# Optimization experiments

Measured on AMD Instinct MI355X. Metric: run time of the kernel, lower is better.

The kernel has to match this reference:

```python
import jax, jax.numpy as jnp
import numpy as np

EPS = 1e-6

def setup_inputs() -> dict:
    key = jax.random.key(0)
    k1, k2, k3 = jax.random.split(key, 3)
    B, N, D = 1, 2048, 1024
    x = jax.random.normal(k1, (B, N, D), dtype=jnp.float32)
    W_qvk = jax.random.normal(k2, (D, 3 * D), dtype=jnp.float32) * (D ** -0.5)
    b_qvk = jax.random.normal(k3, (3 * D,), dtype=jnp.float32) * 0.02
    return {"x": x, "W_qvk": W_qvk, "b_qvk": b_qvk, "head_num": 16}


def _forward(x, W_qvk, b_qvk, head_num):
    B, N, D = x.shape
    qvk = x @ W_qvk + b_qvk                       # (B, N, 3D)
    # torch.chunk order in source: q, v, k
    def to_heads(t):
        return t.reshape(B, N, head_num, D // head_num).transpose(0, 2, 1, 3)  # (B,h,N,e)
    q, v, k = (to_heads(t) for t in jnp.split(qvk, 3, axis=-1))
    e = q.shape[-1]
    # causal linear attention, bucket_size=1
    q = jax.nn.softmax(q, axis=-1) * (e ** -0.5)  # (B,h,N,e)
    k = jnp.exp(k)
    k_cumsum = jnp.cumsum(k, axis=2)              # (B,h,N,e)
    # per-position outer product k_i (x) v_i, then causal prefix-sum over N
    kv = jnp.einsum('bhnd,bhne->bhnde', k, v)     # (B,h,N,e,e)
    kv_cumsum = jnp.cumsum(kv, axis=2)            # (B,h,N,e,e)
    denom = jnp.einsum('bhnd,bhnd->bhn', q, k_cumsum + EPS)   # (B,h,N)
    out = jnp.einsum('bhnd,bhnde->bhne', q, kv_cumsum) / denom[..., None]
    # concat heads: (B,h,N,e) -> (B,N,D)
    return out.transpose(0, 2, 1, 3).reshape(B, N, D)


def reference(x, W_qvk, b_qvk, head_num):
    return _forward(x, W_qvk, b_qvk, head_num)
```

## Files before the change

### kernel.cpp

```cpp
#include <hip/hip_runtime.h>
#include <stdint.h>

#define NTOK 2048
#define NCH 32

typedef __attribute__((ext_vector_type(8))) short bf16x8;
typedef __attribute__((ext_vector_type(8))) unsigned short ushort8v;
typedef __attribute__((ext_vector_type(4))) float f32x4;

__device__ __forceinline__ unsigned short f2bf(float f) {
  unsigned u = __float_as_uint(f);
  u += 0x7fffu + ((u >> 16) & 1u);
  return (unsigned short)(u >> 16);
}
__device__ __forceinline__ float bf2f(unsigned short s) {
  return __uint_as_float(((unsigned)s) << 16);
}

__global__ __launch_bounds__(256) void k_prep_inputs(const float* __restrict__ x,
                                                     unsigned short* __restrict__ xb,
                                                     const float* __restrict__ W,
                                                     unsigned short* __restrict__ Wt) {
  int bid = blockIdx.x;
  if (bid < 2048) {
    int i = (bid * 256 + threadIdx.x) * 4;
    float4 v = *(const float4*)(x + i);
    ushort4 o = { f2bf(v.x), f2bf(v.y), f2bf(v.z), f2bf(v.w) };
    *(ushort4*)(xb + i) = o;
  } else {
    __shared__ float tile[32][33];
    int id = bid - 2048;
    int bx = id % 96, by = id / 96;
    int tx = threadIdx.x & 31, ty = threadIdx.x >> 5;
    int c0 = bx * 32;
    int r0 = by * 32;
#pragma unroll
    for (int j = 0; j < 32; j += 8)
      tile[ty + j][tx] = W[(size_t)(r0 + ty + j) * 3072 + c0 + tx];
    __syncthreads();
#pragma unroll
    for (int j = 0; j < 32; j += 8)
      Wt[(size_t)(c0 + ty + j) * 1024 + r0 + tx] = f2bf(tile[tx][ty + j]);
  }
}

__global__ __launch_bounds__(512, 4) void k_gemm_fused(const unsigned short* __restrict__ xb,
                                                       const unsigned short* __restrict__ wt,
                                                       const float* __restrict__ bias,
                                                       unsigned short* __restrict__ qh,
                                                       unsigned short* __restrict__ kh,
                                                       unsigned short* __restrict__ kt,
                                                       unsigned short* __restrict__ vt) {
  __shared__ __align__(16) unsigned short As[2][128][64];
  __shared__ __align__(16) unsigned short Bs[2][128][64];
  const int t = threadIdx.x;
  const int lane = t & 63;
  const int wave = t >> 6;
  const int wr = wave >> 1;
  const int wc = wave & 1;
  const int rowBase = blockIdx.y * 128;
  const int colBase = blockIdx.x * 128;
  const int fr = lane & 15;
  const int khalf = lane >> 4;

  const int sr = t >> 3;
  const int ssl = (t & 7) ^ (sr & 7);
  const unsigned short* agB = xb + (size_t)(rowBase + sr) * 1024 + ssl * 8;
  const unsigned short* bgB = wt + (size_t)(colBase + sr) * 1024 + ssl * 8;
  char* laB = (char*)As + t * 16;
  char* lbB = (char*)Bs + t * 16;

#define STG(buf, kt0) do {                                                                \
    _Pragma("unroll")                                                                     \
    for (int i_ = 0; i_ < 2; ++i_) {                                                      \
      __builtin_amdgcn_global_load_lds(                                                   \
          (const __attribute__((address_space(1))) void*)(agB + (kt0) * 64 + i_ * 65536), \
          (__attribute__((address_space(3))) void*)(laB + (buf) * 16384 + i_ * 8192), 16, 0, 0); \
      __builtin_amdgcn_global_load_lds(                                                   \
          (const __attribute__((address_space(1))) void*)(bgB + (kt0) * 64 + i_ * 65536), \
          (__attribute__((address_space(3))) void*)(lbB + (buf) * 16384 + i_ * 8192), 16, 0, 0); \
    }                                                                                     \
  } while (0)

#define VMCNT4() asm volatile("s_waitcnt vmcnt(4)" ::: "memory")
#define VMCNT0() asm volatile("s_waitcnt vmcnt(0)" ::: "memory")
#define LGKM0()  asm volatile("s_waitcnt lgkmcnt(0)" ::: "memory")
#define BAR()    __builtin_amdgcn_s_barrier()

  f32x4 acc[2][4] = {};
  const int fs0 = khalf ^ (fr & 7);

#define LOAD_FRAGS(cur, af, bff) do {                                                     \
    _Pragma("unroll")                                                                     \
    for (int m = 0; m < 2; ++m) {                                                         \
      const unsigned short* r = &As[cur][wr * 32 + m * 16 + fr][0];                       \
      af[m][0] = *(const bf16x8*)(r + fs0 * 8);                                           \
      af[m][1] = *(const bf16x8*)(r + (fs0 ^ 4) * 8);                                     \
    }                                                                                     \
    _Pragma("unroll")                                                                     \
    for (int n = 0; n < 4; ++n) {                                                         \
      const unsigned short* r = &Bs[cur][wc * 64 + n * 16 + fr][0];                       \
      bff[n][0] = *(const bf16x8*)(r + fs0 * 8);                                          \
      bff[n][1] = *(const bf16x8*)(r + (fs0 ^ 4) * 8);                                    \
    }                                                                                     \
  } while (0)

#define DO_MFMA(af, bff) do {                                                             \
    _Pragma("unroll")                                                                     \
    for (int m = 0; m < 2; ++m)                                                           \
      _Pragma("unroll")                                                                   \
      for (int n = 0; n < 4; ++n) {                                                       \
        acc[m][n] = __builtin_amdgcn_mfma_f32_16x16x32_bf16(af[m][0], bff[n][0], acc[m][n], 0, 0, 0); \
        acc[m][n] = __builtin_amdgcn_mfma_f32_16x16x32_bf16(af[m][1], bff[n][1], acc[m][n], 0, 0, 0); \
      }                                                                                   \
  } while (0)

  STG(0, 0);
  STG(1, 1);
#pragma unroll 1
  for (int ktile = 0; ktile < 14; ++ktile) {
    const int cur = ktile & 1;
    VMCNT4();
    BAR();
    bf16x8 af[2][2], bff[4][2];
    LOAD_FRAGS(cur, af, bff);
    LGKM0();
    __builtin_amdgcn_sched_barrier(0);
    BAR();
    STG(cur, ktile + 2);
    __builtin_amdgcn_s_setprio(1);
    DO_MFMA(af, bff);
    __builtin_amdgcn_s_setprio(0);
  }
  {
    VMCNT4();
    BAR();
    bf16x8 af[2][2], bff[4][2];
    LOAD_FRAGS(0, af, bff);
    DO_MFMA(af, bff);
  }
  {
    VMCNT0();
    BAR();
    bf16x8 af[2][2], bff[4][2];
    LOAD_FRAGS(1, af, bff);
    DO_MFMA(af, bff);
  }
#undef STG
#undef LOAD_FRAGS
#undef DO_MFMA

  const int g2 = khalf;
  const int ocol = lane & 15;
  const int col0 = colBase + wc * 64;
  const int region = col0 >> 10;
  const int h = (col0 & 1023) >> 6;
  const int r0 = rowBase + wr * 32;
  const int cch = r0 >> 6;
  const int lbase = (wr & 1) * 32;
  float bv[4];
#pragma unroll
  for (int n = 0; n < 4; ++n) bv[n] = bias[col0 + 16 * n + ocol];

  if (region == 0) {
#pragma unroll
    for (int m = 0; m < 2; ++m) {
#pragma unroll
      for (int i = 0; i < 4; ++i) {
        float v[4];
#pragma unroll
        for (int n = 0; n < 4; ++n) v[n] = acc[m][n][i] + bv[n];
        float mx = fmaxf(fmaxf(v[0], v[1]), fmaxf(v[2], v[3]));
#pragma unroll
        for (int off = 1; off <= 8; off <<= 1) mx = fmaxf(mx, __shfl_xor(mx, off));
        float s = 0.f;
#pragma unroll
        for (int n = 0; n < 4; ++n) { v[n] = __expf(v[n] - mx); s += v[n]; }
#pragma unroll
        for (int off = 1; off <= 8; off <<= 1) s += __shfl_xor(s, off);
        float inv = 0.125f / s;
        int tok = r0 + 16 * m + 4 * g2 + i;
        unsigned short* qrow = qh + ((size_t)h * NTOK + tok) * 64;
#pragma unroll
        for (int n = 0; n < 4; ++n) qrow[16 * n + ocol] = f2bf(v[n] * inv);
      }
    }
  } else if (region == 1) {
    unsigned short* vb = vt + (size_t)(h * NCH + cch) * 4096;
#pragma unroll
    for (int m = 0; m < 2; ++m) {
      int tl = lbase + 16 * m + 4 * g2;
#pragma unroll
      for (int n = 0; n < 4; ++n) {
        int e = 16 * n + ocol;
        ushort4 p = { f2bf(acc[m][n][0] + bv[n]), f2bf(acc[m][n][1] + bv[n]),
                      f2bf(acc[m][n][2] + bv[n]), f2bf(acc[m][n][3] + bv[n]) };
        *(ushort4*)&vb[(size_t)e * 64 + tl] = p;
      }
    }
  } else {
    unsigned short* kb = kt + (size_t)(h * NCH + cch) * 4096;
#pragma unroll
    for (int m = 0; m < 2; ++m) {
      int tl = lbase + 16 * m + 4 * g2;
#pragma unroll
      for (int n = 0; n < 4; ++n) {
        int e = 16 * n + ocol;
        float kv[4];
#pragma unroll
        for (int i = 0; i < 4; ++i) kv[i] = __expf(acc[m][n][i] + bv[n]);
        ushort4 p = { f2bf(kv[0]), f2bf(kv[1]), f2bf(kv[2]), f2bf(kv[3]) };
        *(ushort4*)&kb[(size_t)e * 64 + tl] = p;
#pragma unroll
        for (int i = 0; i < 4; ++i)
          kh[((size_t)h * NTOK + r0 + 16 * m + 4 * g2 + i) * 64 + e] = p[i];
      }
    }
  }
}

__global__ __launch_bounds__(256) void k_chunk_sums(const unsigned short* __restrict__ kt,
                                                    const unsigned short* __restrict__ vt,
                                                    float* __restrict__ Sc,
                                                    float* __restrict__ zc) {
  int h = blockIdx.x >> 5, c = blockIdx.x & 31;
  __shared__ __align__(16) unsigned short Kt[64][72], Vt[64][72];
  int t = threadIdx.x, lane = t & 63, w = t >> 6;
  int fr = lane & 15, g = lane >> 4, fko = g * 8;
  const unsigned short* kg = kt + (size_t)(h * NCH + c) * 4096;
  const unsigned short* vg = vt + (size_t)(h * NCH + c) * 4096;
  for (int s = t; s < 512; s += 256) {
    int r = s >> 3, c8 = (s & 7) * 8;
    *(ushort8v*)&Kt[r][c8] = *(const ushort8v*)&kg[r * 64 + c8];
    *(ushort8v*)&Vt[r][c8] = *(const ushort8v*)&vg[r * 64 + c8];
  }
  __syncthreads();
  bf16x8 ka[2];
#pragma unroll
  for (int ks = 0; ks < 2; ++ks) ka[ks] = *(const bf16x8*)&Kt[16 * w + fr][32 * ks + fko];
  f32x4 s4[4] = {};
#pragma unroll
  for (int nb = 0; nb < 4; ++nb)
#pragma unroll
    for (int ks = 0; ks < 2; ++ks) {
      bf16x8 vf = *(const bf16x8*)&Vt[16 * nb + fr][32 * ks + fko];
      s4[nb] = __builtin_amdgcn_mfma_f32_16x16x32_bf16(ka[ks], vf, s4[nb], 0, 0, 0);
    }
  float* so = Sc + (size_t)(h * NCH + c) * 4096;
#pragma unroll
  for (int nb = 0; nb < 4; ++nb) {
    float4 o = { s4[nb][0], s4[nb][1], s4[nb][2], s4[nb][3] };
    *(float4*)&so[(size_t)(16 * nb + fr) * 64 + 16 * w + 4 * g] = o;
  }
  if (w == 0) {
    float z = 0.f;
#pragma unroll
    for (int j = 0; j < 8; ++j) {
      bf16x8 kv = *(const bf16x8*)&Kt[lane][j * 8];
#pragma unroll
      for (int e = 0; e < 8; ++e) z += bf2f((unsigned short)kv[e]);
    }
    zc[(size_t)(h * NCH + c) * 64 + lane] = z;
  }
}

__global__ __launch_bounds__(256) void k_scan(const float* __restrict__ Sc,
                                              unsigned short* __restrict__ Sp,
                                              const float* __restrict__ zc,
                                              float* __restrict__ zp) {
  int b = blockIdx.x;
  if (b < 256) {
    int tg = b * 256 + threadIdx.x;
    int h = tg >> 12, e = tg & 4095;
    float run = 0.f;
    for (int c = 0; c < NCH; ++c) {
      size_t idx = (size_t)(h * NCH + c) * 4096 + e;
      float v = Sc[idx];
      Sp[idx] = f2bf(run);
      run += v;
    }
  } else {
#pragma unroll
    for (int j = 0; j < 4; ++j) {
      int s = threadIdx.x + j * 256;
      int h = s >> 6, d = s & 63;
      float run = 0.f;
      for (int c = 0; c < NCH; ++c) {
        size_t idx = (size_t)(h * NCH + c) * 64 + d;
        zp[idx] = run;
        run += zc[idx];
      }
    }
  }
}

__global__ __launch_bounds__(256) void k_attn(const unsigned short* __restrict__ qh,
                                              const unsigned short* __restrict__ kh,
                                              const unsigned short* __restrict__ vt,
                                              const unsigned short* __restrict__ Sp,
                                              const float* __restrict__ zp,
                                              float* __restrict__ out) {
  int h = blockIdx.x >> 5, c = blockIdx.x & 31;
  __shared__ __align__(16) unsigned short Qs[64][72], Ks[64][72], Vts[64][72], Sts[64][72], Ams[64][72];
  __shared__ float zs[64], denom[64];
  int t = threadIdx.x, lane = t & 63, w = t >> 6;
  int fr = lane & 15, g = lane >> 4, fko = g * 8;
  const unsigned short* qg = qh + ((size_t)h * NTOK + c * 64) * 64;
  const unsigned short* kg = kh + ((size_t)h * NTOK + c * 64) * 64;
  const unsigned short* vg = vt + (size_t)(h * NCH + c) * 4096;
  const unsigned short* sg = Sp + (size_t)(h * NCH + c) * 4096;
  for (int s = t; s < 512; s += 256) {
    int r = s >> 3, c8 = (s & 7) * 8;
    *(ushort8v*)&Qs[r][c8]  = *(const ushort8v*)&qg[r * 64 + c8];
    *(ushort8v*)&Ks[r][c8]  = *(const ushort8v*)&kg[r * 64 + c8];
    *(ushort8v*)&Vts[r][c8] = *(const ushort8v*)&vg[r * 64 + c8];
    *(ushort8v*)&Sts[r][c8] = *(const ushort8v*)&sg[r * 64 + c8];
  }
  if (t < 64) zs[t] = zp[(size_t)(h * NCH + c) * 64 + t];
  __syncthreads();

  bf16x8 qa[2];
#pragma unroll
  for (int ks = 0; ks < 2; ++ks) qa[ks] = *(const bf16x8*)&Qs[16 * w + fr][32 * ks + fko];
  f32x4 a1[4] = {};
#pragma unroll
  for (int mb = 0; mb < 4; ++mb)
#pragma unroll
    for (int ks = 0; ks < 2; ++ks) {
      bf16x8 kf = *(const bf16x8*)&Ks[16 * mb + fr][32 * ks + fko];
      a1[mb] = __builtin_amdgcn_mfma_f32_16x16x32_bf16(qa[ks], kf, a1[mb], 0, 0, 0);
    }
#pragma unroll
  for (int i = 0; i < 4; ++i) {
    int n = 16 * w + 4 * g + i;
    float rs = 0.f;
#pragma unroll
    for (int j = 0; j < 4; ++j) rs += bf2f(Qs[n][fr * 4 + j]) * zs[fr * 4 + j];
#pragma unroll
    for (int mb = 0; mb < 4; ++mb) {
      int m = 16 * mb + fr;
      float v = (m <= n) ? a1[mb][i] : 0.f;
      a1[mb][i] = v;
      rs += v;
      Ams[n][16 * mb + fr] = f2bf(v);
    }
#pragma unroll
    for (int off = 1; off <= 8; off <<= 1) rs += __shfl_xor(rs, off);
    if (fr == 0) denom[n] = rs + 1.25e-7f;
  }
  __syncthreads();

  bf16x8 xa[4];
#pragma unroll
  for (int ks = 0; ks < 2; ++ks) {
    xa[ks]     = *(const bf16x8*)&Vts[16 * w + fr][32 * ks + fko];
    xa[2 + ks] = *(const bf16x8*)&Sts[16 * w + fr][32 * ks + fko];
  }
  f32x4 o4[4] = {};
#pragma unroll
  for (int nb = 0; nb < 4; ++nb)
#pragma unroll
    for (int ks = 0; ks < 2; ++ks) {
      bf16x8 afr = *(const bf16x8*)&Ams[16 * nb + fr][32 * ks + fko];
      o4[nb] = __builtin_amdgcn_mfma_f32_16x16x32_bf16(xa[ks], afr, o4[nb], 0, 0, 0);
      bf16x8 qfr = *(const bf16x8*)&Qs[16 * nb + fr][32 * ks + fko];
      o4[nb] = __builtin_amdgcn_mfma_f32_16x16x32_bf16(xa[2 + ks], qfr, o4[nb], 0, 0, 0);
    }
#pragma unroll
  for (int nb = 0; nb < 4; ++nb) {
    int n = 16 * nb + fr;
    float dv = denom[n];
    float4 res = { o4[nb][0] / dv, o4[nb][1] / dv, o4[nb][2] / dv, o4[nb][3] / dv };
    *(float4*)&out[(size_t)(c * 64 + n) * 1024 + h * 64 + 16 * w + 4 * g] = res;
  }
}

extern "C" void kernel_launch(void* const* d_in, const int* in_sizes, int n_in,
                              void* d_out, int out_size, void* d_ws, size_t ws_size,
                              hipStream_t stream) {
  (void)in_sizes; (void)n_in; (void)out_size; (void)ws_size;
  const float* x = (const float*)d_in[0];
  const float* W = (const float*)d_in[1];
  const float* b = (const float*)d_in[2];
  char* ws = (char*)d_ws;

  const size_t MB = 1024 * 1024;
  unsigned short* xb = (unsigned short*)(ws + 0);
  unsigned short* Wt = (unsigned short*)(ws + 4 * MB);
  unsigned short* qh = (unsigned short*)(ws + 10 * MB);
  unsigned short* kh = (unsigned short*)(ws + 14 * MB);
  unsigned short* kt = (unsigned short*)(ws + 18 * MB);
  unsigned short* vt = (unsigned short*)(ws + 22 * MB);
  float*          Sc = (float*)(ws + 26 * MB);
  unsigned short* Sp = (unsigned short*)(ws + 34 * MB);
  float*          zc = (float*)(ws + 38 * MB);
  float*          zp = (float*)(ws + 38 * MB + 131072);

  k_prep_inputs<<<dim3(5120), dim3(256), 0, stream>>>(x, xb, W, Wt);
  k_gemm_fused<<<dim3(24, 16), dim3(512), 0, stream>>>(xb, Wt, b, qh, kh, kt, vt);
  k_chunk_sums<<<dim3(512), dim3(256), 0, stream>>>(kt, vt, Sc, zc);
  k_scan<<<dim3(257), dim3(256), 0, stream>>>(Sc, Sp, zc, zp);
  k_attn<<<dim3(512), dim3(256), 0, stream>>>(qh, kh, vt, Sp, zp, (float*)d_out);
}
```

Baseline: 48.41 us.

## Fold chunk-state prefix scan into attention kernel and store chunk sums in bf16

Drops the separate k_scan launch. Each attention block now sums the per-chunk KV states and z sums of all earlier chunks itself, reading bf16 chunk sums that k_chunk_sums now writes instead of fp32. This removes one kernel launch and the global round trip for the scanned prefix. In exchange there is redundant O(c) work per block, so later chunks read up to 31 chunk states, which causes load imbalance. Accumulation now happens over values already rounded to bf16, which adds some precision loss.

```diff
diff --git a/kernel.cpp b/kernel.cpp
--- a/kernel.cpp
+++ b/kernel.cpp
@@ -221,7 +221,7 @@
 
 __global__ __launch_bounds__(256) void k_chunk_sums(const unsigned short* __restrict__ kt,
                                                     const unsigned short* __restrict__ vt,
-                                                    float* __restrict__ Sc,
+                                                    unsigned short* __restrict__ Sc,
                                                     float* __restrict__ zc) {
   int h = blockIdx.x >> 5, c = blockIdx.x & 31;
   __shared__ __align__(16) unsigned short Kt[64][72], Vt[64][72];
@@ -246,11 +246,11 @@
       bf16x8 vf = *(const bf16x8*)&Vt[16 * nb + fr][32 * ks + fko];
       s4[nb] = __builtin_amdgcn_mfma_f32_16x16x32_bf16(ka[ks], vf, s4[nb], 0, 0, 0);
     }
-  float* so = Sc + (size_t)(h * NCH + c) * 4096;
+  unsigned short* so = Sc + (size_t)(h * NCH + c) * 4096;
 #pragma unroll
   for (int nb = 0; nb < 4; ++nb) {
-    float4 o = { s4[nb][0], s4[nb][1], s4[nb][2], s4[nb][3] };
-    *(float4*)&so[(size_t)(16 * nb + fr) * 64 + 16 * w + 4 * g] = o;
+    ushort4 o = { f2bf(s4[nb][0]), f2bf(s4[nb][1]), f2bf(s4[nb][2]), f2bf(s4[nb][3]) };
+    *(ushort4*)&so[(size_t)(16 * nb + fr) * 64 + 16 * w + 4 * g] = o;
   }
   if (w == 0) {
     float z = 0.f;
@@ -261,44 +261,14 @@
       for (int e = 0; e < 8; ++e) z += bf2f((unsigned short)kv[e]);
     }
     zc[(size_t)(h * NCH + c) * 64 + lane] = z;
-  }
-}
-
-__global__ __launch_bounds__(256) void k_scan(const float* __restrict__ Sc,
-                                              unsigned short* __restrict__ Sp,
-                                              const float* __restrict__ zc,
-                                              float* __restrict__ zp) {
-  int b = blockIdx.x;
-  if (b < 256) {
-    int tg = b * 256 + threadIdx.x;
-    int h = tg >> 12, e = tg & 4095;
-    float run = 0.f;
-    for (int c = 0; c < NCH; ++c) {
-      size_t idx = (size_t)(h * NCH + c) * 4096 + e;
-      float v = Sc[idx];
-      Sp[idx] = f2bf(run);
-      run += v;
-    }
-  } else {
-#pragma unroll
-    for (int j = 0; j < 4; ++j) {
-      int s = threadIdx.x + j * 256;
-      int h = s >> 6, d = s & 63;
-      float run = 0.f;
-      for (int c = 0; c < NCH; ++c) {
-        size_t idx = (size_t)(h * NCH + c) * 64 + d;
-        zp[idx] = run;
-        run += zc[idx];
-      }
-    }
   }
 }
 
 __global__ __launch_bounds__(256) void k_attn(const unsigned short* __restrict__ qh,
                                               const unsigned short* __restrict__ kh,
                                               const unsigned short* __restrict__ vt,
-                                              const unsigned short* __restrict__ Sp,
-                                              const float* __restrict__ zp,
+                                              const unsigned short* __restrict__ Sc,
+                                              const float* __restrict__ zc,
                                               float* __restrict__ out) {
   int h = blockIdx.x >> 5, c = blockIdx.x & 31;
   __shared__ __align__(16) unsigned short Qs[64][72], Ks[64][72], Vts[64][72], Sts[64][72], Ams[64][72];
@@ -308,15 +278,33 @@
   const unsigned short* qg = qh + ((size_t)h * NTOK + c * 64) * 64;
   const unsigned short* kg = kh + ((size_t)h * NTOK + c * 64) * 64;
   const unsigned short* vg = vt + (size_t)(h * NCH + c) * 4096;
-  const unsigned short* sg = Sp + (size_t)(h * NCH + c) * 4096;
   for (int s = t; s < 512; s += 256) {
     int r = s >> 3, c8 = (s & 7) * 8;
     *(ushort8v*)&Qs[r][c8]  = *(const ushort8v*)&qg[r * 64 + c8];
     *(ushort8v*)&Ks[r][c8]  = *(const ushort8v*)&kg[r * 64 + c8];
     *(ushort8v*)&Vts[r][c8] = *(const ushort8v*)&vg[r * 64 + c8];
-    *(ushort8v*)&Sts[r][c8] = *(const ushort8v*)&sg[r * 64 + c8];
-  }
-  if (t < 64) zs[t] = zp[(size_t)(h * NCH + c) * 64 + t];
+  }
+  {
+    float r[16] = {};
+    const unsigned short* sb = Sc + ((size_t)h * NCH) * 4096 + t * 16;
+    for (int cc = 0; cc < c; ++cc) {
+      ushort8v u0 = *(const ushort8v*)(sb + (size_t)cc * 4096);
+      ushort8v u1 = *(const ushort8v*)(sb + (size_t)cc * 4096 + 8);
+#pragma unroll
+      for (int j = 0; j < 8; ++j) { r[j] += bf2f(u0[j]); r[8 + j] += bf2f(u1[j]); }
+    }
+    ushort8v o0, o1;
+#pragma unroll
+    for (int j = 0; j < 8; ++j) { o0[j] = f2bf(r[j]); o1[j] = f2bf(r[8 + j]); }
+    int rr = t >> 2, ccol = (t & 3) * 16;
+    *(ushort8v*)&Sts[rr][ccol] = o0;
+    *(ushort8v*)&Sts[rr][ccol + 8] = o1;
+  }
+  if (t < 64) {
+    float z = 0.f;
+    for (int cc = 0; cc < c; ++cc) z += zc[((size_t)h * NCH + cc) * 64 + t];
+    zs[t] = z;
+  }
   __syncthreads();
 
   bf16x8 qa[2];
@@ -391,14 +379,11 @@
   unsigned short* kh = (unsigned short*)(ws + 14 * MB);
   unsigned short* kt = (unsigned short*)(ws + 18 * MB);
   unsigned short* vt = (unsigned short*)(ws + 22 * MB);
-  float*          Sc = (float*)(ws + 26 * MB);
-  unsigned short* Sp = (unsigned short*)(ws + 34 * MB);
-  float*          zc = (float*)(ws + 38 * MB);
-  float*          zp = (float*)(ws + 38 * MB + 131072);
+  unsigned short* Sc = (unsigned short*)(ws + 26 * MB);
+  float*          zc = (float*)(ws + 30 * MB);
 
   k_prep_inputs<<<dim3(5120), dim3(256), 0, stream>>>(x, xb, W, Wt);
   k_gemm_fused<<<dim3(24, 16), dim3(512), 0, stream>>>(xb, Wt, b, qh, kh, kt, vt);
   k_chunk_sums<<<dim3(512), dim3(256), 0, stream>>>(kt, vt, Sc, zc);
-  k_scan<<<dim3(257), dim3(256), 0, stream>>>(Sc, Sp, zc, zp);
-  k_attn<<<dim3(512), dim3(256), 0, stream>>>(qh, kh, vt, Sp, zp, (float*)d_out);
-}
+  k_attn<<<dim3(512), dim3(256), 0, stream>>>(qh, kh, vt, Sc, zc, (float*)d_out);
+}
```

Result: slower. 56.30 us (+16.3%).

## Fuse chunk-sum, scan and attention into one cooperative kernel with grid syncs

Applied to the files above, without the earlier changes.

Merges the three tail kernels (per-chunk KV sums, cross-chunk prefix scan, and chunked attention) into one cooperative kernel that uses grid-wide barriers in place of kernel boundaries. The per-chunk KV sums are now stored as bf16 instead of fp32, which halves that intermediate traffic. The aim is to remove two launch gaps and shrink memory traffic. In exchange it requires all 512 blocks to be co-resident, rounds the chunk sums to bf16 before the scan, and leaves most blocks idle during the scan phase.

```diff
diff --git a/kernel.cpp b/kernel.cpp
--- a/kernel.cpp
+++ b/kernel.cpp
@@ -1,5 +1,8 @@
 #include <hip/hip_runtime.h>
+#include <hip/hip_cooperative_groups.h>
 #include <stdint.h>
+
+namespace cg = cooperative_groups;
 
 #define NTOK 2048
 #define NCH 32
@@ -219,92 +222,88 @@
   }
 }
 
-__global__ __launch_bounds__(256) void k_chunk_sums(const unsigned short* __restrict__ kt,
-                                                    const unsigned short* __restrict__ vt,
-                                                    float* __restrict__ Sc,
-                                                    float* __restrict__ zc) {
-  int h = blockIdx.x >> 5, c = blockIdx.x & 31;
-  __shared__ __align__(16) unsigned short Kt[64][72], Vt[64][72];
-  int t = threadIdx.x, lane = t & 63, w = t >> 6;
-  int fr = lane & 15, g = lane >> 4, fko = g * 8;
-  const unsigned short* kg = kt + (size_t)(h * NCH + c) * 4096;
-  const unsigned short* vg = vt + (size_t)(h * NCH + c) * 4096;
-  for (int s = t; s < 512; s += 256) {
-    int r = s >> 3, c8 = (s & 7) * 8;
-    *(ushort8v*)&Kt[r][c8] = *(const ushort8v*)&kg[r * 64 + c8];
-    *(ushort8v*)&Vt[r][c8] = *(const ushort8v*)&vg[r * 64 + c8];
-  }
-  __syncthreads();
-  bf16x8 ka[2];
-#pragma unroll
-  for (int ks = 0; ks < 2; ++ks) ka[ks] = *(const bf16x8*)&Kt[16 * w + fr][32 * ks + fko];
-  f32x4 s4[4] = {};
-#pragma unroll
-  for (int nb = 0; nb < 4; ++nb)
-#pragma unroll
-    for (int ks = 0; ks < 2; ++ks) {
-      bf16x8 vf = *(const bf16x8*)&Vt[16 * nb + fr][32 * ks + fko];
-      s4[nb] = __builtin_amdgcn_mfma_f32_16x16x32_bf16(ka[ks], vf, s4[nb], 0, 0, 0);
-    }
-  float* so = Sc + (size_t)(h * NCH + c) * 4096;
-#pragma unroll
-  for (int nb = 0; nb < 4; ++nb) {
-    float4 o = { s4[nb][0], s4[nb][1], s4[nb][2], s4[nb][3] };
-    *(float4*)&so[(size_t)(16 * nb + fr) * 64 + 16 * w + 4 * g] = o;
-  }
-  if (w == 0) {
-    float z = 0.f;
-#pragma unroll
-    for (int j = 0; j < 8; ++j) {
-      bf16x8 kv = *(const bf16x8*)&Kt[lane][j * 8];
-#pragma unroll
-      for (int e = 0; e < 8; ++e) z += bf2f((unsigned short)kv[e]);
-    }
-    zc[(size_t)(h * NCH + c) * 64 + lane] = z;
-  }
-}
-
-__global__ __launch_bounds__(256) void k_scan(const float* __restrict__ Sc,
-                                              unsigned short* __restrict__ Sp,
-                                              const float* __restrict__ zc,
-                                              float* __restrict__ zp) {
-  int b = blockIdx.x;
-  if (b < 256) {
-    int tg = b * 256 + threadIdx.x;
-    int h = tg >> 12, e = tg & 4095;
-    float run = 0.f;
-    for (int c = 0; c < NCH; ++c) {
-      size_t idx = (size_t)(h * NCH + c) * 4096 + e;
-      float v = Sc[idx];
-      Sp[idx] = f2bf(run);
-      run += v;
-    }
-  } else {
-#pragma unroll
-    for (int j = 0; j < 4; ++j) {
-      int s = threadIdx.x + j * 256;
-      int h = s >> 6, d = s & 63;
-      float run = 0.f;
-      for (int c = 0; c < NCH; ++c) {
-        size_t idx = (size_t)(h * NCH + c) * 64 + d;
-        zp[idx] = run;
-        run += zc[idx];
-      }
-    }
-  }
-}
-
-__global__ __launch_bounds__(256) void k_attn(const unsigned short* __restrict__ qh,
-                                              const unsigned short* __restrict__ kh,
-                                              const unsigned short* __restrict__ vt,
-                                              const unsigned short* __restrict__ Sp,
-                                              const float* __restrict__ zp,
-                                              float* __restrict__ out) {
-  int h = blockIdx.x >> 5, c = blockIdx.x & 31;
+__global__ __launch_bounds__(256, 3) void k_tail(const unsigned short* __restrict__ kt,
+                                                 const unsigned short* __restrict__ vt,
+                                                 unsigned short* __restrict__ Sc,
+                                                 float* __restrict__ zc,
+                                                 unsigned short* __restrict__ Sp,
+                                                 float* __restrict__ zp,
+                                                 const unsigned short* __restrict__ qh,
+                                                 const unsigned short* __restrict__ kh,
+                                                 float* __restrict__ out) {
   __shared__ __align__(16) unsigned short Qs[64][72], Ks[64][72], Vts[64][72], Sts[64][72], Ams[64][72];
   __shared__ float zs[64], denom[64];
-  int t = threadIdx.x, lane = t & 63, w = t >> 6;
-  int fr = lane & 15, g = lane >> 4, fko = g * 8;
+  const int h = blockIdx.x >> 5, c = blockIdx.x & 31;
+  const int t = threadIdx.x, lane = t & 63, w = t >> 6;
+  const int fr = lane & 15, g = lane >> 4, fko = g * 8;
+
+  {
+    const unsigned short* kg = kt + (size_t)(h * NCH + c) * 4096;
+    const unsigned short* vg = vt + (size_t)(h * NCH + c) * 4096;
+    for (int s = t; s < 512; s += 256) {
+      int r = s >> 3, c8 = (s & 7) * 8;
+      *(ushort8v*)&Qs[r][c8] = *(const ushort8v*)&kg[r * 64 + c8];
+      *(ushort8v*)&Ks[r][c8] = *(const ushort8v*)&vg[r * 64 + c8];
+    }
+    __syncthreads();
+    bf16x8 ka[2];
+#pragma unroll
+    for (int ks = 0; ks < 2; ++ks) ka[ks] = *(const bf16x8*)&Qs[16 * w + fr][32 * ks + fko];
+    f32x4 s4[4] = {};
+#pragma unroll
+    for (int nb = 0; nb < 4; ++nb)
+#pragma unroll
+      for (int ks = 0; ks < 2; ++ks) {
+        bf16x8 vf = *(const bf16x8*)&Ks[16 * nb + fr][32 * ks + fko];
+        s4[nb] = __builtin_amdgcn_mfma_f32_16x16x32_bf16(ka[ks], vf, s4[nb], 0, 0, 0);
+      }
+    unsigned short* so = Sc + (size_t)(h * NCH + c) * 4096;
+#pragma unroll
+    for (int nb = 0; nb < 4; ++nb) {
+      ushort4 o = { f2bf(s4[nb][0]), f2bf(s4[nb][1]), f2bf(s4[nb][2]), f2bf(s4[nb][3]) };
+      *(ushort4*)&so[(size_t)(16 * nb + fr) * 64 + 16 * w + 4 * g] = o;
+    }
+    if (w == 0) {
+      float z = 0.f;
+#pragma unroll
+      for (int j = 0; j < 8; ++j) {
+        bf16x8 kv = *(const bf16x8*)&Qs[lane][j * 8];
+#pragma unroll
+        for (int e = 0; e < 8; ++e) z += bf2f((unsigned short)kv[e]);
+      }
+      zc[(size_t)(h * NCH + c) * 64 + lane] = z;
+    }
+  }
+  cg::this_grid().sync();
+
+  {
+    int b = blockIdx.x;
+    if (b < 256) {
+      int tg = b * 256 + t;
+      int hh = tg >> 12, e = tg & 4095;
+      float run = 0.f;
+      for (int cc = 0; cc < NCH; ++cc) {
+        size_t idx = (size_t)(hh * NCH + cc) * 4096 + e;
+        float v = bf2f(Sc[idx]);
+        Sp[idx] = f2bf(run);
+        run += v;
+      }
+    } else if (b == 256) {
+#pragma unroll
+      for (int j = 0; j < 4; ++j) {
+        int s = t + j * 256;
+        int hh = s >> 6, d = s & 63;
+        float run = 0.f;
+        for (int cc = 0; cc < NCH; ++cc) {
+          size_t idx = (size_t)(hh * NCH + cc) * 64 + d;
+          zp[idx] = run;
+          run += zc[idx];
+        }
+      }
+    }
+  }
+  cg::this_grid().sync();
+
   const unsigned short* qg = qh + ((size_t)h * NTOK + c * 64) * 64;
   const unsigned short* kg = kh + ((size_t)h * NTOK + c * 64) * 64;
   const unsigned short* vg = vt + (size_t)(h * NCH + c) * 4096;
@@ -391,14 +390,16 @@
   unsigned short* kh = (unsigned short*)(ws + 14 * MB);
   unsigned short* kt = (unsigned short*)(ws + 18 * MB);
   unsigned short* vt = (unsigned short*)(ws + 22 * MB);
-  float*          Sc = (float*)(ws + 26 * MB);
-  unsigned short* Sp = (unsigned short*)(ws + 34 * MB);
-  float*          zc = (float*)(ws + 38 * MB);
-  float*          zp = (float*)(ws + 38 * MB + 131072);
+  unsigned short* Sc = (unsigned short*)(ws + 26 * MB);
+  unsigned short* Sp = (unsigned short*)(ws + 30 * MB);
+  float*          zc = (float*)(ws + 34 * MB);
+  float*          zp = (float*)(ws + 34 * MB + 131072);
+  float*          outf = (float*)d_out;
 
   k_prep_inputs<<<dim3(5120), dim3(256), 0, stream>>>(x, xb, W, Wt);
   k_gemm_fused<<<dim3(24, 16), dim3(512), 0, stream>>>(xb, Wt, b, qh, kh, kt, vt);
-  k_chunk_sums<<<dim3(512), dim3(256), 0, stream>>>(kt, vt, Sc, zc);
-  k_scan<<<dim3(257), dim3(256), 0, stream>>>(Sc, Sp, zc, zp);
-  k_attn<<<dim3(512), dim3(256), 0, stream>>>(qh, kh, vt, Sp, zp, (float*)d_out);
-}
+
+  void* args[] = { (void*)&kt, (void*)&vt, (void*)&Sc, (void*)&zc,
+                   (void*)&Sp, (void*)&zp, (void*)&qh, (void*)&kh, (void*)&outf };
+  hipLaunchCooperativeKernel((const void*)k_tail, dim3(512), dim3(256), args, 0, stream);
+}
```

New measurement: 164.6 us. 3.4x slower.

## Widen GEMM tile to 128x192 with 12 waves and split A/B staging

Applied to the files above, without the earlier changes.

Enlarges the QKV projection GEMM block tile from 128x128 to 128x192 using 768 threads (12 waves in a 4x3 layout). The grid shrinks to 256 blocks, one per CU. Global-to-LDS staging is split so the first 256 threads load A and the remaining 512 load B, with per-group vmcnt waits. The aim is better operand reuse and a single balanced wave of blocks, at the cost of lower occupancy and more LDS per block. The epilogue was not visibly adapted to the wider column tile, so output mapping correctness is uncertain.

```diff
diff --git a/kernel.cpp b/kernel.cpp
--- a/kernel.cpp
+++ b/kernel.cpp
@@ -44,7 +44,7 @@
   }
 }
 
-__global__ __launch_bounds__(512, 4) void k_gemm_fused(const unsigned short* __restrict__ xb,
+__global__ __launch_bounds__(768, 1) void k_gemm_fused(const unsigned short* __restrict__ xb,
                                                        const unsigned short* __restrict__ wt,
                                                        const float* __restrict__ bias,
                                                        unsigned short* __restrict__ qh,
@@ -52,37 +52,46 @@
                                                        unsigned short* __restrict__ kt,
                                                        unsigned short* __restrict__ vt) {
   __shared__ __align__(16) unsigned short As[2][128][64];
-  __shared__ __align__(16) unsigned short Bs[2][128][64];
+  __shared__ __align__(16) unsigned short Bs[2][192][64];
   const int t = threadIdx.x;
   const int lane = t & 63;
   const int wave = t >> 6;
-  const int wr = wave >> 1;
-  const int wc = wave & 1;
+  const int wr = wave / 3;
+  const int wc = wave % 3;
   const int rowBase = blockIdx.y * 128;
-  const int colBase = blockIdx.x * 128;
+  const int colBase = blockIdx.x * 192;
   const int fr = lane & 15;
   const int khalf = lane >> 4;
 
-  const int sr = t >> 3;
-  const int ssl = (t & 7) ^ (sr & 7);
-  const unsigned short* agB = xb + (size_t)(rowBase + sr) * 1024 + ssl * 8;
-  const unsigned short* bgB = wt + (size_t)(colBase + sr) * 1024 + ssl * 8;
-  char* laB = (char*)As + t * 16;
-  char* lbB = (char*)Bs + t * 16;
+  const bool isA = t < 256;
+  const int nL = isA ? 4 : 3;
+  const int bstr = isA ? 16384 : 24576;
+  const unsigned short* gsrc[4];
+  char* ldst[4];
+#pragma unroll
+  for (int j = 0; j < 4; ++j) {
+    int idx = isA ? (t + j * 256) : (t - 256 + j * 512);
+    if (j >= nL) idx = 0;
+    int row = idx >> 3;
+    int ssl = (idx & 7) ^ (row & 7);
+    gsrc[j] = (isA ? xb + (size_t)(rowBase + row) * 1024
+                   : wt + (size_t)(colBase + row) * 1024) + ssl * 8;
+    ldst[j] = (isA ? (char*)As : (char*)Bs) + idx * 16;
+  }
 
 #define STG(buf, kt0) do {                                                                \
     _Pragma("unroll")                                                                     \
-    for (int i_ = 0; i_ < 2; ++i_) {                                                      \
-      __builtin_amdgcn_global_load_lds(                                                   \
-          (const __attribute__((address_space(1))) void*)(agB + (kt0) * 64 + i_ * 65536), \
-          (__attribute__((address_space(3))) void*)(laB + (buf) * 16384 + i_ * 8192), 16, 0, 0); \
-      __builtin_amdgcn_global_load_lds(                                                   \
-          (const __attribute__((address_space(1))) void*)(bgB + (kt0) * 64 + i_ * 65536), \
-          (__attribute__((address_space(3))) void*)(lbB + (buf) * 16384 + i_ * 8192), 16, 0, 0); \
-    }                                                                                     \
+    for (int j_ = 0; j_ < 4; ++j_)                                                        \
+      if (j_ < nL)                                                                        \
+        __builtin_amdgcn_global_load_lds(                                                 \
+            (const __attribute__((address_space(1))) void*)(gsrc[j_] + (kt0) * 64),       \
+            (__attribute__((address_space(3))) void*)(ldst[j_] + (buf) * bstr), 16, 0, 0);\
   } while (0)
 
-#define VMCNT4() asm volatile("s_waitcnt vmcnt(4)" ::: "memory")
+#define VMW_STEADY() do {                                                                 \
+    if (isA) asm volatile("s_waitcnt vmcnt(4)" ::: "memory");                             \
+    else     asm volatile("s_waitcnt vmcnt(3)" ::: "memory");                             \
+  } while (0)
 #define VMCNT0() asm volatile("s_waitcnt vmcnt(0)" ::: "memory")
 #define LGKM0()  asm volatile("s_waitcnt lgkmcnt(0)" ::: "memory")
 #define BAR()    __builtin_amdgcn_s_barrier()
@@ -120,7 +129,7 @@
 #pragma unroll 1
   for (int ktile = 0; ktile < 14; ++ktile) {
     const int cur = ktile & 1;
-    VMCNT4();
+    VMW_STEADY();
     BAR();
     bf16x8 af[2][2], bff[4][2];
     LOAD_FRAGS(cur, af, bff);
@@ -133,7 +142,7 @@
     __builtin_amdgcn_s_setprio(0);
   }
   {
-    VMCNT4();
+    VMW_STEADY();
     BAR();
     bf16x8 af[2][2], bff[4][2];
     LOAD_FRAGS(0, af, bff);
@@ -397,7 +406,7 @@
   float*          zp = (float*)(ws + 38 * MB + 131072);
 
   k_prep_inputs<<<dim3(5120), dim3(256), 0, stream>>>(x, xb, W, Wt);
-  k_gemm_fused<<<dim3(24, 16), dim3(512), 0, stream>>>(xb, Wt, b, qh, kh, kt, vt);
+  k_gemm_fused<<<dim3(16, 16), dim3(768), 0, stream>>>(xb, Wt, b, qh, kh, kt, vt);
   k_chunk_sums<<<dim3(512), dim3(256), 0, stream>>>(kt, vt, Sc, zc);
   k_scan<<<dim3(257), dim3(256), 0, stream>>>(Sc, Sp, zc, zp);
   k_attn<<<dim3(512), dim3(256), 0, stream>>>(qh, kh, vt, Sp, zp, (float*)d_out);
```

Measured after the change: 48.41 us. Within noise of the previous version (+0.0%).
